# Optimization experiments

Measured on AMD Instinct MI355X. Metric: run time of the kernel, lower is better.

Reference implementation:

```python
import jax, jax.numpy as jnp
import numpy as np

N_NODES = 50000
N_EDGES = 800000
D_N = 64      # node feature dim
D_E = 64      # edge feature dim
HID = 128     # MLP hidden dim
D_OUT = 64    # edge/node MLP output dim


def _mlp_params(key, d_in, d_hid, d_out):
    k1, k2 = jax.random.split(key)
    s1 = 1.0 / np.sqrt(d_in)
    s2 = 1.0 / np.sqrt(d_hid)
    return (
        jax.random.uniform(k1, (d_in, d_hid), jnp.float32, -s1, s1),
        jnp.zeros((d_hid,), jnp.float32),
        jax.random.uniform(k2, (d_hid, d_out), jnp.float32, -s2, s2),
        jnp.zeros((d_out,), jnp.float32),
    )


def setup_inputs() -> dict:
    key = jax.random.key(0)
    ks = jax.random.split(key, 7)
    nf = jax.random.normal(ks[0], (N_NODES, D_N), jnp.float32)
    ef = jax.random.normal(ks[1], (N_EDGES, D_E), jnp.float32)
    src = jax.random.randint(ks[2], (N_EDGES,), 0, N_NODES, jnp.int64)
    dst = jax.random.randint(ks[3], (N_EDGES,), 0, N_NODES, jnp.int64)
    We1, be1, We2, be2 = _mlp_params(ks[4], 2 * D_N + D_E, HID, D_OUT)
    Wa1, ba1, Wa2, ba2 = _mlp_params(ks[5], 2 * D_N + D_E, HID, D_OUT)
    Wn1, bn1, Wn2, bn2 = _mlp_params(ks[6], D_OUT + D_N, HID, D_OUT)
    return dict(nf=nf, ef=ef, src=src, dst=dst,
                We1=We1, be1=be1, We2=We2, be2=be2,
                Wa1=Wa1, ba1=ba1, Wa2=Wa2, ba2=ba2,
                Wn1=Wn1, bn1=bn1, Wn2=Wn2, bn2=bn2)


def _mlp(x, W1, b1, W2, b2):
    return jax.nn.relu(x @ W1 + b1) @ W2 + b2


def reference(nf, ef, src, dst,
              We1, be1, We2, be2,
              Wa1, ba1, Wa2, ba2,
              Wn1, bn1, Wn2, bn2):
    # edge update: gather src/dst node feats, concat with edge feats  [E, 2*D_N + D_E]
    x_e = jnp.concatenate([nf[src], nf[dst], ef], axis=-1)
    e_out = _mlp(x_e, We1, be1, We2, be2)                 # [E, D_OUT]
    gate = jax.nn.sigmoid(_mlp(x_e, Wa1, ba1, Wa2, ba2))  # [E, D_OUT]
    updated_ef = gate * e_out                              # message m == updated edge feat
    # scatter-sum messages into destination nodes
    agg_m = jax.ops.segment_sum(updated_ef, dst, num_segments=N_NODES)  # [N, D_OUT]
    # node update
    x_n = jnp.concatenate([agg_m, nf], axis=-1)            # [N, D_OUT + D_N]
    updated_nf = _mlp(x_n, Wn1, bn1, Wn2, bn2)             # [N, D_OUT]
    return updated_nf, updated_ef
```

## Files before the change

### kernel.cpp

```cpp
#include <hip/hip_runtime.h>

#define NN 50000
#define NE 800000

typedef float f32x4 __attribute__((ext_vector_type(4)));
typedef short s16x8 __attribute__((ext_vector_type(8)));
typedef unsigned short u16;

__device__ __forceinline__ u16 f2bf(float f) {
  union { float f; unsigned u; } v; v.f = f;
  unsigned r = v.u + 0x7FFFu + ((v.u >> 16) & 1u);
  return (u16)(r >> 16);
}

__device__ __forceinline__ void st_bf4(u16* p, f32x4 v) {
  ushort4 pv;
  pv.x = f2bf(v.x); pv.y = f2bf(v.y); pv.z = f2bf(v.z); pv.w = f2bf(v.w);
  *(ushort4*)p = pv;
}

__global__ void zero_kernel(f32x4* __restrict__ p) {
  f32x4 z; z[0] = 0.f; z[1] = 0.f; z[2] = 0.f; z[3] = 0.f;
  p[(size_t)blockIdx.x * 256 + threadIdx.x] = z;
}

__device__ __forceinline__ void pack_one(const float* __restrict__ W, int N,
                                         u16* __restrict__ out, int t) {
  int j = t & 7, lane = (t >> 3) & 63, f = t >> 9;
  int NT = N >> 4;
  int nt = f % NT, ks = f / NT;
  int row = ks * 32 + ((lane >> 4) << 3) + j;
  int col = nt * 16 + (lane & 15);
  out[t] = f2bf(W[row * N + col]);
}

__global__ void pack_kernel(const float* __restrict__ We1, const float* __restrict__ We2,
                            const float* __restrict__ Wa1, const float* __restrict__ Wa2,
                            const float* __restrict__ Wn1, const float* __restrict__ Wn2,
                            u16* __restrict__ out) {
  int t = blockIdx.x * 256 + threadIdx.x;
  if (t < 24576)      pack_one(We1, 128, out,          t);
  else if (t < 32768) pack_one(We2, 64,  out + 24576,  t - 24576);
  else if (t < 57344) pack_one(Wa1, 128, out + 32768,  t - 32768);
  else if (t < 65536) pack_one(Wa2, 64,  out + 57344,  t - 57344);
  else if (t < 81920) pack_one(Wn1, 128, out + 65536,  t - 65536);
  else if (t < 90112) pack_one(Wn2, 64,  out + 81920,  t - 81920);
}

__global__ __launch_bounds__(256, 2)
void edge_kernel(const float* __restrict__ nf, const float* __restrict__ ef,
                 const int* __restrict__ src, const int* __restrict__ dst,
                 const u16* __restrict__ W1e, const float* __restrict__ b1e,
                 const u16* __restrict__ W2e, const float* __restrict__ b2e,
                 const u16* __restrict__ W1a, const float* __restrict__ b1a,
                 const u16* __restrict__ W2a, const float* __restrict__ b2a,
                 float* __restrict__ out_ef, float* __restrict__ agg) {
  __shared__ u16 xe[4][16 * 200];
  __shared__ u16 hs[4][16 * 136];
  __shared__ int sdst[4][16];
  const int w = threadIdx.x >> 6, lane = threadIdx.x & 63;
  const int e0 = blockIdx.x * 64 + w * 16;
  const int er = lane >> 4, c4 = (lane & 15) * 4;

  #pragma unroll
  for (int g = 0; g < 4; ++g) {
    int el = g * 4 + er;
    int e = e0 + el;
    int s = src[e], d = dst[e];
    if (c4 == 0) sdst[w][el] = d;
    f32x4 fs = *(const f32x4*)(nf + (size_t)s * 64 + c4);
    f32x4 fd = *(const f32x4*)(nf + (size_t)d * 64 + c4);
    f32x4 fe = *(const f32x4*)(ef + (size_t)e * 64 + c4);
    u16* row = &xe[w][el * 200];
    st_bf4(row + c4, fs);
    st_bf4(row + 64 + c4, fd);
    st_bf4(row + 128 + c4, fe);
  }
  __syncthreads();

  const int m = lane & 15, q = lane >> 4;
  s16x8 a1[6];
  #pragma unroll
  for (int k = 0; k < 6; ++k)
    a1[k] = *(const s16x8*)&xe[w][m * 200 + k * 32 + q * 8];

  f32x4 acc[8];
  #pragma unroll
  for (int i = 0; i < 8; ++i) { acc[i][0] = 0.f; acc[i][1] = 0.f; acc[i][2] = 0.f; acc[i][3] = 0.f; }
  #pragma unroll
  for (int nt = 0; nt < 8; ++nt)
    #pragma unroll
    for (int k = 0; k < 6; ++k) {
      s16x8 b = *(const s16x8*)(W1e + ((size_t)(k * 8 + nt) * 64 + lane) * 8);
      acc[nt] = __builtin_amdgcn_mfma_f32_16x16x32_bf16(a1[k], b, acc[nt], 0, 0, 0);
    }
  #pragma unroll
  for (int nt = 0; nt < 8; ++nt) {
    float bv = b1e[nt * 16 + m];
    #pragma unroll
    for (int r = 0; r < 4; ++r) {
      float h = acc[nt][r] + bv;
      h = h > 0.f ? h : 0.f;
      hs[w][(q * 4 + r) * 136 + nt * 16 + m] = f2bf(h);
    }
  }
  __syncthreads();

  s16x8 a2[4];
  #pragma unroll
  for (int k = 0; k < 4; ++k)
    a2[k] = *(const s16x8*)&hs[w][m * 136 + k * 32 + q * 8];
  f32x4 eo[4];
  #pragma unroll
  for (int i = 0; i < 4; ++i) { eo[i][0] = 0.f; eo[i][1] = 0.f; eo[i][2] = 0.f; eo[i][3] = 0.f; }
  #pragma unroll
  for (int nt = 0; nt < 4; ++nt)
    #pragma unroll
    for (int k = 0; k < 4; ++k) {
      s16x8 b = *(const s16x8*)(W2e + ((size_t)(k * 4 + nt) * 64 + lane) * 8);
      eo[nt] = __builtin_amdgcn_mfma_f32_16x16x32_bf16(a2[k], b, eo[nt], 0, 0, 0);
    }

  f32x4 accg[8];
  #pragma unroll
  for (int i = 0; i < 8; ++i) { accg[i][0] = 0.f; accg[i][1] = 0.f; accg[i][2] = 0.f; accg[i][3] = 0.f; }
  #pragma unroll
  for (int nt = 0; nt < 8; ++nt)
    #pragma unroll
    for (int k = 0; k < 6; ++k) {
      s16x8 b = *(const s16x8*)(W1a + ((size_t)(k * 8 + nt) * 64 + lane) * 8);
      accg[nt] = __builtin_amdgcn_mfma_f32_16x16x32_bf16(a1[k], b, accg[nt], 0, 0, 0);
    }
  __syncthreads();
  #pragma unroll
  for (int nt = 0; nt < 8; ++nt) {
    float bv = b1a[nt * 16 + m];
    #pragma unroll
    for (int r = 0; r < 4; ++r) {
      float h = accg[nt][r] + bv;
      h = h > 0.f ? h : 0.f;
      hs[w][(q * 4 + r) * 136 + nt * 16 + m] = f2bf(h);
    }
  }
  __syncthreads();

  s16x8 a2g[4];
  #pragma unroll
  for (int k = 0; k < 4; ++k)
    a2g[k] = *(const s16x8*)&hs[w][m * 136 + k * 32 + q * 8];
  f32x4 go[4];
  #pragma unroll
  for (int i = 0; i < 4; ++i) { go[i][0] = 0.f; go[i][1] = 0.f; go[i][2] = 0.f; go[i][3] = 0.f; }
  #pragma unroll
  for (int nt = 0; nt < 4; ++nt)
    #pragma unroll
    for (int k = 0; k < 4; ++k) {
      s16x8 b = *(const s16x8*)(W2a + ((size_t)(k * 4 + nt) * 64 + lane) * 8);
      go[nt] = __builtin_amdgcn_mfma_f32_16x16x32_bf16(a2g[k], b, go[nt], 0, 0, 0);
    }

  #pragma unroll
  for (int nt = 0; nt < 4; ++nt) {
    int col = nt * 16 + m;
    float be2v = b2e[col], ba2v = b2a[col];
    #pragma unroll
    for (int r = 0; r < 4; ++r) {
      int rowi = q * 4 + r;
      int e = e0 + rowi;
      float ev = eo[nt][r] + be2v;
      float gv = go[nt][r] + ba2v;
      float gs = 1.f / (1.f + __expf(-gv));
      float val = gs * ev;
      out_ef[(size_t)e * 64 + col] = val;
      atomicAdd(agg + (size_t)sdst[w][rowi] * 64 + col, val);
    }
  }
}

__global__ __launch_bounds__(256, 2)
void node_kernel(const float* __restrict__ nf, const float* __restrict__ agg,
                 const u16* __restrict__ W1n, const float* __restrict__ b1n,
                 const u16* __restrict__ W2n, const float* __restrict__ b2n,
                 float* __restrict__ out_nf) {
  __shared__ u16 xn[4][16 * 136];
  __shared__ u16 hn[4][16 * 136];
  const int w = threadIdx.x >> 6, lane = threadIdx.x & 63;
  const int n0 = blockIdx.x * 64 + w * 16;
  const int er = lane >> 4, c4 = (lane & 15) * 4;

  #pragma unroll
  for (int g = 0; g < 4; ++g) {
    int nl = g * 4 + er;
    int n = n0 + nl; if (n >= NN) n = NN - 1;
    f32x4 fa = *(const f32x4*)(agg + (size_t)n * 64 + c4);
    f32x4 fn = *(const f32x4*)(nf + (size_t)n * 64 + c4);
    u16* row = &xn[w][nl * 136];
    st_bf4(row + c4, fa);
    st_bf4(row + 64 + c4, fn);
  }
  __syncthreads();

  const int m = lane & 15, q = lane >> 4;
  s16x8 a1[4];
  #pragma unroll
  for (int k = 0; k < 4; ++k)
    a1[k] = *(const s16x8*)&xn[w][m * 136 + k * 32 + q * 8];
  f32x4 acc[8];
  #pragma unroll
  for (int i = 0; i < 8; ++i) { acc[i][0] = 0.f; acc[i][1] = 0.f; acc[i][2] = 0.f; acc[i][3] = 0.f; }
  #pragma unroll
  for (int nt = 0; nt < 8; ++nt)
    #pragma unroll
    for (int k = 0; k < 4; ++k) {
      s16x8 b = *(const s16x8*)(W1n + ((size_t)(k * 8 + nt) * 64 + lane) * 8);
      acc[nt] = __builtin_amdgcn_mfma_f32_16x16x32_bf16(a1[k], b, acc[nt], 0, 0, 0);
    }
  #pragma unroll
  for (int nt = 0; nt < 8; ++nt) {
    float bv = b1n[nt * 16 + m];
    #pragma unroll
    for (int r = 0; r < 4; ++r) {
      float h = acc[nt][r] + bv;
      h = h > 0.f ? h : 0.f;
      hn[w][(q * 4 + r) * 136 + nt * 16 + m] = f2bf(h);
    }
  }
  __syncthreads();

  s16x8 a2[4];
  #pragma unroll
  for (int k = 0; k < 4; ++k)
    a2[k] = *(const s16x8*)&hn[w][m * 136 + k * 32 + q * 8];
  f32x4 o[4];
  #pragma unroll
  for (int i = 0; i < 4; ++i) { o[i][0] = 0.f; o[i][1] = 0.f; o[i][2] = 0.f; o[i][3] = 0.f; }
  #pragma unroll
  for (int nt = 0; nt < 4; ++nt)
    #pragma unroll
    for (int k = 0; k < 4; ++k) {
      s16x8 b = *(const s16x8*)(W2n + ((size_t)(k * 4 + nt) * 64 + lane) * 8);
      o[nt] = __builtin_amdgcn_mfma_f32_16x16x32_bf16(a2[k], b, o[nt], 0, 0, 0);
    }
  #pragma unroll
  for (int nt = 0; nt < 4; ++nt) {
    int col = nt * 16 + m;
    float bv = b2n[col];
    #pragma unroll
    for (int r = 0; r < 4; ++r) {
      int rowi = q * 4 + r;
      int n = n0 + rowi;
      if (n < NN) out_nf[(size_t)n * 64 + col] = o[nt][r] + bv;
    }
  }
}

extern "C" void kernel_launch(void* const* d_in, const int* in_sizes, int n_in,
                              void* d_out, int out_size, void* d_ws, size_t ws_size,
                              hipStream_t stream) {
  const float* nf  = (const float*)d_in[0];
  const float* ef  = (const float*)d_in[1];
  const int*   src = (const int*)d_in[2];
  const int*   dst = (const int*)d_in[3];
  const float* We1 = (const float*)d_in[4];
  const float* be1 = (const float*)d_in[5];
  const float* We2 = (const float*)d_in[6];
  const float* be2 = (const float*)d_in[7];
  const float* Wa1 = (const float*)d_in[8];
  const float* ba1 = (const float*)d_in[9];
  const float* Wa2 = (const float*)d_in[10];
  const float* ba2 = (const float*)d_in[11];
  const float* Wn1 = (const float*)d_in[12];
  const float* bn1 = (const float*)d_in[13];
  const float* Wn2 = (const float*)d_in[14];
  const float* bn2 = (const float*)d_in[15];
  float* out = (float*)d_out;
  float* agg = (float*)d_ws;
  u16* pk = (u16*)((char*)d_ws + (size_t)NN * 64 * 4);

  zero_kernel<<<3125, 256, 0, stream>>>((f32x4*)agg);
  pack_kernel<<<352, 256, 0, stream>>>(We1, We2, Wa1, Wa2, Wn1, Wn2, pk);
  edge_kernel<<<NE / 64, 256, 0, stream>>>(nf, ef, src, dst,
      pk, be1, pk + 24576, be2, pk + 32768, ba1, pk + 57344, ba2,
      out + (size_t)NN * 64, agg);
  node_kernel<<<(NN + 63) / 64, 256, 0, stream>>>(nf, agg,
      pk + 65536, bn1, pk + 81920, bn2, out);
}
```

Before: 723.9 us.

## Replace block barriers with wave-local fences, alias LDS buffers, raise occupancy

Each wave only touches its own LDS slice, so the block-wide __syncthreads calls are replaced with compiler memory fences. The input and hidden LDS buffers are merged into one per-wave region, and launch bounds rise to 4 blocks per CU to allow more waves in flight. The zeroing kernel becomes hipMemsetAsync. The risks are that a compiler-only fence does not wait for outstanding LDS operations within the wave (correctness rests on in-order LDS execution within a wave), and that the higher occupancy target may force register spills given the large MFMA accumulator arrays.

```diff
diff --git a/kernel.cpp b/kernel.cpp
--- a/kernel.cpp
+++ b/kernel.cpp
@@ -6,6 +6,8 @@
 typedef float f32x4 __attribute__((ext_vector_type(4)));
 typedef short s16x8 __attribute__((ext_vector_type(8)));
 typedef unsigned short u16;
+
+#define WAVE_FENCE() asm volatile("" ::: "memory")
 
 __device__ __forceinline__ u16 f2bf(float f) {
   union { float f; unsigned u; } v; v.f = f;
@@ -17,11 +19,6 @@
   ushort4 pv;
   pv.x = f2bf(v.x); pv.y = f2bf(v.y); pv.z = f2bf(v.z); pv.w = f2bf(v.w);
   *(ushort4*)p = pv;
-}
-
-__global__ void zero_kernel(f32x4* __restrict__ p) {
-  f32x4 z; z[0] = 0.f; z[1] = 0.f; z[2] = 0.f; z[3] = 0.f;
-  p[(size_t)blockIdx.x * 256 + threadIdx.x] = z;
 }
 
 __device__ __forceinline__ void pack_one(const float* __restrict__ W, int N,
@@ -47,7 +44,7 @@
   else if (t < 90112) pack_one(Wn2, 64,  out + 81920,  t - 81920);
 }
 
-__global__ __launch_bounds__(256, 2)
+__global__ __launch_bounds__(256, 4)
 void edge_kernel(const float* __restrict__ nf, const float* __restrict__ ef,
                  const int* __restrict__ src, const int* __restrict__ dst,
                  const u16* __restrict__ W1e, const float* __restrict__ b1e,
@@ -55,12 +52,13 @@
                  const u16* __restrict__ W1a, const float* __restrict__ b1a,
                  const u16* __restrict__ W2a, const float* __restrict__ b2a,
                  float* __restrict__ out_ef, float* __restrict__ agg) {
-  __shared__ u16 xe[4][16 * 200];
-  __shared__ u16 hs[4][16 * 136];
+  __shared__ u16 buf[4][16 * 200];
   __shared__ int sdst[4][16];
   const int w = threadIdx.x >> 6, lane = threadIdx.x & 63;
   const int e0 = blockIdx.x * 64 + w * 16;
   const int er = lane >> 4, c4 = (lane & 15) * 4;
+  u16* const xe = buf[w];
+  u16* const hs = buf[w];
 
   #pragma unroll
   for (int g = 0; g < 4; ++g) {
@@ -71,18 +69,19 @@
     f32x4 fs = *(const f32x4*)(nf + (size_t)s * 64 + c4);
     f32x4 fd = *(const f32x4*)(nf + (size_t)d * 64 + c4);
     f32x4 fe = *(const f32x4*)(ef + (size_t)e * 64 + c4);
-    u16* row = &xe[w][el * 200];
+    u16* row = xe + el * 200;
     st_bf4(row + c4, fs);
     st_bf4(row + 64 + c4, fd);
     st_bf4(row + 128 + c4, fe);
   }
-  __syncthreads();
+  WAVE_FENCE();
 
   const int m = lane & 15, q = lane >> 4;
   s16x8 a1[6];
   #pragma unroll
   for (int k = 0; k < 6; ++k)
-    a1[k] = *(const s16x8*)&xe[w][m * 200 + k * 32 + q * 8];
+    a1[k] = *(const s16x8*)(xe + m * 200 + k * 32 + q * 8);
+  WAVE_FENCE();
 
   f32x4 acc[8];
   #pragma unroll
@@ -101,15 +100,15 @@
     for (int r = 0; r < 4; ++r) {
       float h = acc[nt][r] + bv;
       h = h > 0.f ? h : 0.f;
-      hs[w][(q * 4 + r) * 136 + nt * 16 + m] = f2bf(h);
-    }
-  }
-  __syncthreads();
+      hs[(q * 4 + r) * 136 + nt * 16 + m] = f2bf(h);
+    }
+  }
+  WAVE_FENCE();
 
   s16x8 a2[4];
   #pragma unroll
   for (int k = 0; k < 4; ++k)
-    a2[k] = *(const s16x8*)&hs[w][m * 136 + k * 32 + q * 8];
+    a2[k] = *(const s16x8*)(hs + m * 136 + k * 32 + q * 8);
   f32x4 eo[4];
   #pragma unroll
   for (int i = 0; i < 4; ++i) { eo[i][0] = 0.f; eo[i][1] = 0.f; eo[i][2] = 0.f; eo[i][3] = 0.f; }
@@ -131,7 +130,7 @@
       s16x8 b = *(const s16x8*)(W1a + ((size_t)(k * 8 + nt) * 64 + lane) * 8);
       accg[nt] = __builtin_amdgcn_mfma_f32_16x16x32_bf16(a1[k], b, accg[nt], 0, 0, 0);
     }
-  __syncthreads();
+  WAVE_FENCE();
   #pragma unroll
   for (int nt = 0; nt < 8; ++nt) {
     float bv = b1a[nt * 16 + m];
@@ -139,15 +138,15 @@
     for (int r = 0; r < 4; ++r) {
       float h = accg[nt][r] + bv;
       h = h > 0.f ? h : 0.f;
-      hs[w][(q * 4 + r) * 136 + nt * 16 + m] = f2bf(h);
-    }
-  }
-  __syncthreads();
+      hs[(q * 4 + r) * 136 + nt * 16 + m] = f2bf(h);
+    }
+  }
+  WAVE_FENCE();
 
   s16x8 a2g[4];
   #pragma unroll
   for (int k = 0; k < 4; ++k)
-    a2g[k] = *(const s16x8*)&hs[w][m * 136 + k * 32 + q * 8];
+    a2g[k] = *(const s16x8*)(hs + m * 136 + k * 32 + q * 8);
   f32x4 go[4];
   #pragma unroll
   for (int i = 0; i < 4; ++i) { go[i][0] = 0.f; go[i][1] = 0.f; go[i][2] = 0.f; go[i][3] = 0.f; }
@@ -177,16 +176,17 @@
   }
 }
 
-__global__ __launch_bounds__(256, 2)
+__global__ __launch_bounds__(256, 4)
 void node_kernel(const float* __restrict__ nf, const float* __restrict__ agg,
                  const u16* __restrict__ W1n, const float* __restrict__ b1n,
                  const u16* __restrict__ W2n, const float* __restrict__ b2n,
                  float* __restrict__ out_nf) {
-  __shared__ u16 xn[4][16 * 136];
-  __shared__ u16 hn[4][16 * 136];
+  __shared__ u16 buf[4][16 * 136];
   const int w = threadIdx.x >> 6, lane = threadIdx.x & 63;
   const int n0 = blockIdx.x * 64 + w * 16;
   const int er = lane >> 4, c4 = (lane & 15) * 4;
+  u16* const xn = buf[w];
+  u16* const hn = buf[w];
 
   #pragma unroll
   for (int g = 0; g < 4; ++g) {
@@ -194,17 +194,19 @@
     int n = n0 + nl; if (n >= NN) n = NN - 1;
     f32x4 fa = *(const f32x4*)(agg + (size_t)n * 64 + c4);
     f32x4 fn = *(const f32x4*)(nf + (size_t)n * 64 + c4);
-    u16* row = &xn[w][nl * 136];
+    u16* row = xn + nl * 136;
     st_bf4(row + c4, fa);
     st_bf4(row + 64 + c4, fn);
   }
-  __syncthreads();
+  WAVE_FENCE();
 
   const int m = lane & 15, q = lane >> 4;
   s16x8 a1[4];
   #pragma unroll
   for (int k = 0; k < 4; ++k)
-    a1[k] = *(const s16x8*)&xn[w][m * 136 + k * 32 + q * 8];
+    a1[k] = *(const s16x8*)(xn + m * 136 + k * 32 + q * 8);
+  WAVE_FENCE();
+
   f32x4 acc[8];
   #pragma unroll
   for (int i = 0; i < 8; ++i) { acc[i][0] = 0.f; acc[i][1] = 0.f; acc[i][2] = 0.f; acc[i][3] = 0.f; }
@@ -222,15 +224,15 @@
     for (int r = 0; r < 4; ++r) {
       float h = acc[nt][r] + bv;
       h = h > 0.f ? h : 0.f;
-      hn[w][(q * 4 + r) * 136 + nt * 16 + m] = f2bf(h);
-    }
-  }
-  __syncthreads();
+      hn[(q * 4 + r) * 136 + nt * 16 + m] = f2bf(h);
+    }
+  }
+  WAVE_FENCE();
 
   s16x8 a2[4];
   #pragma unroll
   for (int k = 0; k < 4; ++k)
-    a2[k] = *(const s16x8*)&hn[w][m * 136 + k * 32 + q * 8];
+    a2[k] = *(const s16x8*)(hn + m * 136 + k * 32 + q * 8);
   f32x4 o[4];
   #pragma unroll
   for (int i = 0; i < 4; ++i) { o[i][0] = 0.f; o[i][1] = 0.f; o[i][2] = 0.f; o[i][3] = 0.f; }
@@ -277,7 +279,7 @@
   float* agg = (float*)d_ws;
   u16* pk = (u16*)((char*)d_ws + (size_t)NN * 64 * 4);
 
-  zero_kernel<<<3125, 256, 0, stream>>>((f32x4*)agg);
+  hipMemsetAsync(agg, 0, (size_t)NN * 64 * 4, stream);
   pack_kernel<<<352, 256, 0, stream>>>(We1, We2, Wa1, Wa2, Wn1, Wn2, pk);
   edge_kernel<<<NE / 64, 256, 0, stream>>>(nf, ef, src, dst,
       pk, be1, pk + 24576, be2, pk + 32768, ba1, pk + 57344, ba2,
```

Result: slower. 858.0 us (+18.5%).

## Replace atomic scatter-add with CSR gather aggregation in node kernel

Applied to the files above, without the earlier changes.

Builds a CSR index of edges grouped by destination node on every call, using count, single-block scan and fill kernels. The node kernel then sums the messages of each node by gathering rows of out_ef, so the edge kernel no longer issues 51.2M float atomics into agg. The cost is four extra launches, a serial single-block scan, integer atomics, and scattered random reads of messages in the node kernel. Occupancy hints on the edge and node kernels are also raised.

```diff
diff --git a/kernel.cpp b/kernel.cpp
--- a/kernel.cpp
+++ b/kernel.cpp
@@ -17,11 +17,6 @@
   ushort4 pv;
   pv.x = f2bf(v.x); pv.y = f2bf(v.y); pv.z = f2bf(v.z); pv.w = f2bf(v.w);
   *(ushort4*)p = pv;
-}
-
-__global__ void zero_kernel(f32x4* __restrict__ p) {
-  f32x4 z; z[0] = 0.f; z[1] = 0.f; z[2] = 0.f; z[3] = 0.f;
-  p[(size_t)blockIdx.x * 256 + threadIdx.x] = z;
 }
 
 __device__ __forceinline__ void pack_one(const float* __restrict__ W, int N,
@@ -47,17 +42,76 @@
   else if (t < 90112) pack_one(Wn2, 64,  out + 81920,  t - 81920);
 }
 
-__global__ __launch_bounds__(256, 2)
+
+__global__ void count_kernel(const int* __restrict__ dst, int* __restrict__ cnt) {
+  int e = blockIdx.x * 256 + threadIdx.x;
+  if (e < NE) atomicAdd(cnt + dst[e], 1);
+}
+
+__global__ __launch_bounds__(1024)
+void scan_kernel(const int* __restrict__ cnt, int* __restrict__ off,
+                 int* __restrict__ cursor) {
+  const int CHUNK = 49;
+  const int t = threadIdx.x;
+  const int i0 = t * CHUNK;
+  int local = 0;
+  for (int k = 0; k < CHUNK; ++k) {
+    int i = i0 + k;
+    if (i < NN) local += cnt[i];
+  }
+  const int lane = t & 63, wv = t >> 6;
+  int s = local;
+  #pragma unroll
+  for (int d = 1; d < 64; d <<= 1) {
+    int u = __shfl_up(s, d, 64);
+    if (lane >= d) s += u;
+  }
+  __shared__ int wsum[16];
+  if (lane == 63) wsum[wv] = s;
+  __syncthreads();
+  if (t < 16) {
+    int ws = wsum[t];
+    #pragma unroll
+    for (int d = 1; d < 16; d <<= 1) {
+      int u = __shfl_up(ws, d, 64);
+      if (t >= d) ws += u;
+    }
+    wsum[t] = ws;
+  }
+  __syncthreads();
+  int base = (wv > 0 ? wsum[wv - 1] : 0) + (s - local);
+  int run = base;
+  for (int k = 0; k < CHUNK; ++k) {
+    int i = i0 + k;
+    if (i < NN) {
+      off[i] = run;
+      cursor[i] = run;
+      run += cnt[i];
+    }
+  }
+  if (t == 1023) off[NN] = run;
+}
+
+__global__ void fill_kernel(const int* __restrict__ dst, int* __restrict__ cursor,
+                            int* __restrict__ eidx) {
+  int e = blockIdx.x * 256 + threadIdx.x;
+  if (e < NE) {
+    int slot = atomicAdd(cursor + dst[e], 1);
+    eidx[slot] = e;
+  }
+}
+
+
+__global__ __launch_bounds__(256, 3)
 void edge_kernel(const float* __restrict__ nf, const float* __restrict__ ef,
                  const int* __restrict__ src, const int* __restrict__ dst,
                  const u16* __restrict__ W1e, const float* __restrict__ b1e,
                  const u16* __restrict__ W2e, const float* __restrict__ b2e,
                  const u16* __restrict__ W1a, const float* __restrict__ b1a,
                  const u16* __restrict__ W2a, const float* __restrict__ b2a,
-                 float* __restrict__ out_ef, float* __restrict__ agg) {
+                 float* __restrict__ out_ef) {
   __shared__ u16 xe[4][16 * 200];
   __shared__ u16 hs[4][16 * 136];
-  __shared__ int sdst[4][16];
   const int w = threadIdx.x >> 6, lane = threadIdx.x & 63;
   const int e0 = blockIdx.x * 64 + w * 16;
   const int er = lane >> 4, c4 = (lane & 15) * 4;
@@ -67,7 +121,6 @@
     int el = g * 4 + er;
     int e = e0 + el;
     int s = src[e], d = dst[e];
-    if (c4 == 0) sdst[w][el] = d;
     f32x4 fs = *(const f32x4*)(nf + (size_t)s * 64 + c4);
     f32x4 fd = *(const f32x4*)(nf + (size_t)d * 64 + c4);
     f32x4 fe = *(const f32x4*)(ef + (size_t)e * 64 + c4);
@@ -165,20 +218,19 @@
     float be2v = b2e[col], ba2v = b2a[col];
     #pragma unroll
     for (int r = 0; r < 4; ++r) {
-      int rowi = q * 4 + r;
-      int e = e0 + rowi;
+      int e = e0 + q * 4 + r;
       float ev = eo[nt][r] + be2v;
       float gv = go[nt][r] + ba2v;
       float gs = 1.f / (1.f + __expf(-gv));
-      float val = gs * ev;
-      out_ef[(size_t)e * 64 + col] = val;
-      atomicAdd(agg + (size_t)sdst[w][rowi] * 64 + col, val);
-    }
-  }
-}
-
-__global__ __launch_bounds__(256, 2)
-void node_kernel(const float* __restrict__ nf, const float* __restrict__ agg,
+      out_ef[(size_t)e * 64 + col] = gs * ev;
+    }
+  }
+}
+
+
+__global__ __launch_bounds__(256, 4)
+void node_kernel(const float* __restrict__ nf, const float* __restrict__ msg,
+                 const int* __restrict__ off, const int* __restrict__ eidx,
                  const u16* __restrict__ W1n, const float* __restrict__ b1n,
                  const u16* __restrict__ W2n, const float* __restrict__ b2n,
                  float* __restrict__ out_nf) {
@@ -192,11 +244,16 @@
   for (int g = 0; g < 4; ++g) {
     int nl = g * 4 + er;
     int n = n0 + nl; if (n >= NN) n = NN - 1;
-    f32x4 fa = *(const f32x4*)(agg + (size_t)n * 64 + c4);
-    f32x4 fn = *(const f32x4*)(nf + (size_t)n * 64 + c4);
+    int beg = off[n], end = off[n + 1];
+    f32x4 s; s[0] = 0.f; s[1] = 0.f; s[2] = 0.f; s[3] = 0.f;
+    for (int i = beg; i < end; ++i) {
+      int e = eidx[i];
+      s += *(const f32x4*)(msg + (size_t)e * 64 + c4);
+    }
+    f32x4 fn4 = *(const f32x4*)(nf + (size_t)n * 64 + c4);
     u16* row = &xn[w][nl * 136];
-    st_bf4(row + c4, fa);
-    st_bf4(row + 64 + c4, fn);
+    st_bf4(row + c4, s);
+    st_bf4(row + 64 + c4, fn4);
   }
   __syncthreads();
 
@@ -247,8 +304,7 @@
     float bv = b2n[col];
     #pragma unroll
     for (int r = 0; r < 4; ++r) {
-      int rowi = q * 4 + r;
-      int n = n0 + rowi;
+      int n = n0 + q * 4 + r;
       if (n < NN) out_nf[(size_t)n * 64 + col] = o[nt][r] + bv;
     }
   }
@@ -274,14 +330,23 @@
   const float* Wn2 = (const float*)d_in[14];
   const float* bn2 = (const float*)d_in[15];
   float* out = (float*)d_out;
-  float* agg = (float*)d_ws;
-  u16* pk = (u16*)((char*)d_ws + (size_t)NN * 64 * 4);
-
-  zero_kernel<<<3125, 256, 0, stream>>>((f32x4*)agg);
+  float* out_ef = out + (size_t)NN * 64;
+
+  char* ws = (char*)d_ws;
+  u16* pk     = (u16*)ws;
+  int* cnt    = (int*)(ws + 180224);
+  int* off    = (int*)(ws + 380224);
+  int* cursor = (int*)(ws + 580240);
+  int* eidx   = (int*)(ws + 780240);
+
+  hipMemsetAsync(cnt, 0, (size_t)NN * sizeof(int), stream);
   pack_kernel<<<352, 256, 0, stream>>>(We1, We2, Wa1, Wa2, Wn1, Wn2, pk);
+  count_kernel<<<(NE + 255) / 256, 256, 0, stream>>>(dst, cnt);
+  scan_kernel<<<1, 1024, 0, stream>>>(cnt, off, cursor);
+  fill_kernel<<<(NE + 255) / 256, 256, 0, stream>>>(dst, cursor, eidx);
   edge_kernel<<<NE / 64, 256, 0, stream>>>(nf, ef, src, dst,
       pk, be1, pk + 24576, be2, pk + 32768, ba1, pk + 57344, ba2,
-      out + (size_t)NN * 64, agg);
-  node_kernel<<<(NN + 63) / 64, 256, 0, stream>>>(nf, agg,
+      out_ef);
+  node_kernel<<<(NN + 63) / 64, 256, 0, stream>>>(nf, out_ef, off, eidx,
       pk + 65536, bn1, pk + 81920, bn2, out);
 }
```

Result: slower. 872.4 us (+20.5%).
